# Optimization experiments

Measured on AMD Instinct MI355X. Metric: run time of the kernel, lower is better.

The kernel has to match this reference:

```python
import jax, jax.numpy as jnp
import numpy as np

B, T, C, H = 4, 2048, 1024, 16
HD = C // H  # head dim = 64


def setup_inputs() -> dict:
    key = jax.random.key(0)
    k1, k2, k3 = jax.random.split(key, 3)
    scale_in = 1.0 / np.sqrt(C)
    return {
        "x": jax.random.normal(k1, (B, T, C), dtype=jnp.float32),
        "W_attn": jax.random.normal(k2, (C, 3 * C), dtype=jnp.float32) * scale_in,
        "b_attn": jnp.zeros((3 * C,), dtype=jnp.float32),
        "W_proj": jax.random.normal(k3, (C, C), dtype=jnp.float32) * scale_in,
        "b_proj": jnp.zeros((C,), dtype=jnp.float32),
    }


def reference(x, W_attn, b_attn, W_proj, b_proj):
    b, t, c = x.shape
    qkv = x @ W_attn + b_attn                      # [B,T,3C]
    q, k, v = jnp.split(qkv, 3, axis=-1)
    # [B,T,C] -> [B,H,T,HD]
    def heads(z):
        return z.reshape(b, t, H, HD).transpose(0, 2, 1, 3)
    q, k, v = heads(q), heads(k), heads(v)
    att = jnp.einsum("bhqd,bhkd->bhqk", q, k) / jnp.sqrt(jnp.float32(HD))
    causal = jnp.tril(jnp.ones((t, t), dtype=bool))
    att = jnp.where(causal, att, -jnp.inf)
    att = jax.nn.softmax(att, axis=-1)             # dropout p=0 -> identity
    y = jnp.einsum("bhqk,bhkd->bhqd", att, v)      # [B,H,T,HD]
    y = y.transpose(0, 2, 1, 3).reshape(b, t, c)   # [B,T,C]
    return y @ W_proj + b_proj
```

## Files before the change

kernel.cpp:

```cpp
#include <hip/hip_runtime.h>
#include <hip/hip_bf16.h>

typedef unsigned int u32;
typedef unsigned short u16;
typedef __bf16 bf16x8 __attribute__((ext_vector_type(8)));
typedef float f32x4 __attribute__((ext_vector_type(4)));
typedef _Float16 f16;
typedef _Float16 f16x2 __attribute__((ext_vector_type(2)));
typedef _Float16 f16x4 __attribute__((ext_vector_type(4)));

#define B_ 4
#define T_ 2048
#define C_ 1024
#define H_ 16
#define HD_ 64
#define M_ (B_*T_)
#define N3C (3*C_)
#define N2C (2*C_)

__device__ __forceinline__ u16 f2bf(float f) {
  u32 u = __builtin_bit_cast(u32, f);
  u = (u + 0x7fffu + ((u >> 16) & 1u)) >> 16;
  return (u16)u;
}

#define GLD16(gp, lp) __builtin_amdgcn_global_load_lds( \
    (const __attribute__((address_space(1))) u32*)(gp), \
    (__attribute__((address_space(3))) u32*)(lp), 16, 0, 0)

#if __has_builtin(__builtin_amdgcn_exp2f)
#define EXP2F(x) __builtin_amdgcn_exp2f(x)
#else
#define EXP2F(x) exp2f(x)
#endif

__global__ __launch_bounds__(256) void prep(
    const float* __restrict__ x, const float* __restrict__ Wa,
    const float* __restrict__ Wp,
    u16* __restrict__ xb, u16* __restrict__ W1t, u16* __restrict__ W2t) {
  __shared__ float t[32][33];
  const int blk = blockIdx.x, tid = threadIdx.x;
  if (blk < 8192) {
    int i = blk * 256 + tid;
    float4 v = ((const float4*)x)[i];
    ushort4 o;
    o.x = f2bf(v.x); o.y = f2bf(v.y); o.z = f2bf(v.z); o.w = f2bf(v.w);
    ((ushort4*)xb)[i] = o;
    return;
  }
  const float* W; u16* Wt; int Ndim, id;
  if (blk < 8192 + 3072) { W = Wa; Wt = W1t; Ndim = N3C; id = blk - 8192; }
  else                   { W = Wp; Wt = W2t; Ndim = C_;  id = blk - 11264; }
  const int nt = Ndim / 32;
  const int n0 = (id % nt) * 32, k0 = (id / nt) * 32;
  const int tx = tid & 31, ty = tid >> 5;
  #pragma unroll
  for (int i = ty; i < 32; i += 8)
    t[i][tx] = W[(long)(k0 + i) * Ndim + n0 + tx];
  __syncthreads();
  #pragma unroll
  for (int i = ty; i < 32; i += 8)
    Wt[(long)(n0 + i) * C_ + k0 + tx] = f2bf(t[tx][i]);
}

__global__ __launch_bounds__(256) void gemm_qkv(
    const u16* __restrict__ A, const u16* __restrict__ Bt,
    const float* __restrict__ bias, u16* __restrict__ qkout,
    f16* __restrict__ vt) {
  __shared__ u16 As[128 * 64];
  __shared__ u16 Bs[128 * 64];
  const int tid = threadIdx.x;
  const int wave = tid >> 6, lane = tid & 63;
  const int wm = wave >> 1, wn = wave & 1;
  const int l15 = lane & 15, quad = lane >> 4;
  const int rA = lane >> 3, cxor = (lane & 7) ^ rA;
  const long rowA0 = (long)blockIdx.x * 128;
  const long colB0 = (long)blockIdx.y * 128;
  const int K = C_;

  f32x4 acc[4][4] = {};

  const u16* Ag = A + (rowA0 + wave * 32 + rA) * K + cxor * 8;
  const u16* Bg = Bt + (colB0 + wave * 32 + rA) * K + cxor * 8;
  u16* Asw = &As[(wave * 32) * 64];
  u16* Bsw = &Bs[(wave * 32) * 64];

  const int fbase = l15 * 64 + ((quad ^ (l15 & 3)) << 3) + (((l15 >> 2) & 1) << 5);
  const int aA0 = wm * 4096 + fbase, aA1 = aA0 ^ 32;
  const int bA0 = wn * 4096 + fbase, bA1 = bA0 ^ 32;

  for (int k0 = 0; k0 < K; k0 += 64) {
    #pragma unroll
    for (int j = 0; j < 4; ++j) {
      GLD16(Ag + (long)j * 8 * K + k0, Asw + j * 8 * 64);
      GLD16(Bg + (long)j * 8 * K + k0, Bsw + j * 8 * 64);
    }
    __syncthreads();
    #pragma unroll
    for (int kk = 0; kk < 2; ++kk) {
      const int ai = kk ? aA1 : aA0;
      const int bi = kk ? bA1 : bA0;
      bf16x8 af[4], bfr[4];
      #pragma unroll
      for (int mt = 0; mt < 4; ++mt)
        af[mt] = *(const bf16x8*)&As[ai + mt * 1024];
      #pragma unroll
      for (int nt = 0; nt < 4; ++nt)
        bfr[nt] = *(const bf16x8*)&Bs[bi + nt * 1024];
      #pragma unroll
      for (int mt = 0; mt < 4; ++mt)
        #pragma unroll
        for (int nt = 0; nt < 4; ++nt)
          acc[mt][nt] = __builtin_amdgcn_mfma_f32_16x16x32_bf16(
              af[mt], bfr[nt], acc[mt][nt], 0, 0, 0);
    }
    __syncthreads();
  }

  float bl[4];
  #pragma unroll
  for (int nt = 0; nt < 4; ++nt)
    bl[nt] = bias[colB0 + wn * 64 + nt * 16 + l15];

  const bool vmode = (colB0 >= N2C);
  #pragma unroll
  for (int mt = 0; mt < 4; ++mt) {
    long row = rowA0 + wm * 64 + mt * 16 + quad * 4;
    #pragma unroll
    for (int nt = 0; nt < 4; ++nt) {
      long col = colB0 + wn * 64 + nt * 16 + l15;
      float v0 = acc[mt][nt][0] + bl[nt];
      float v1 = acc[mt][nt][1] + bl[nt];
      float v2 = acc[mt][nt][2] + bl[nt];
      float v3 = acc[mt][nt][3] + bl[nt];
      if (!vmode) {
        qkout[(row + 0) * N2C + col] = f2bf(v0);
        qkout[(row + 1) * N2C + col] = f2bf(v1);
        qkout[(row + 2) * N2C + col] = f2bf(v2);
        qkout[(row + 3) * N2C + col] = f2bf(v3);
      } else {
        int cv = (int)(col - N2C);
        int hh = cv >> 6, dd = cv & 63;
        int bb = (int)(row >> 11);
        long t = row & 2047;
        f16x2 lo = __builtin_bit_cast(f16x2, __builtin_amdgcn_cvt_pkrtz(v0, v1));
        f16x2 hi = __builtin_bit_cast(f16x2, __builtin_amdgcn_cvt_pkrtz(v2, v3));
        f16x4 w; w[0] = lo[0]; w[1] = lo[1]; w[2] = hi[0]; w[3] = hi[1];
        *(f16x4*)&vt[(((long)bb * H_ + hh) * HD_ + dd) * T_ + t] = w;
      }
    }
  }
}

__global__ __launch_bounds__(256) void gemm_proj(
    const u16* __restrict__ A, const u16* __restrict__ Bt,
    const float* __restrict__ bias, float* __restrict__ Cout) {
  __shared__ u16 As[128 * 64];
  __shared__ u16 Bs[64 * 64];
  const int tid = threadIdx.x;
  const int wave = tid >> 6, lane = tid & 63;
  const int l15 = lane & 15, quad = lane >> 4;
  const int rA = lane >> 3, cxor = (lane & 7) ^ rA;
  const long rowA0 = (long)blockIdx.x * 128;
  const long colB0 = (long)blockIdx.y * 64;
  const int K = C_;

  f32x4 acc[2][4] = {};

  const u16* Ag = A + (rowA0 + wave * 32 + rA) * K + cxor * 8;
  const u16* Bg = Bt + (colB0 + wave * 16 + rA) * K + cxor * 8;
  u16* Asw = &As[(wave * 32) * 64];
  u16* Bsw = &Bs[(wave * 16) * 64];

  const int fbase = l15 * 64 + ((quad ^ (l15 & 3)) << 3) + (((l15 >> 2) & 1) << 5);
  const int aA0 = wave * 2048 + fbase, aA1 = aA0 ^ 32;
  const int bA0 = fbase, bA1 = bA0 ^ 32;

  for (int k0 = 0; k0 < K; k0 += 64) {
    #pragma unroll
    for (int j = 0; j < 4; ++j)
      GLD16(Ag + (long)j * 8 * K + k0, Asw + j * 8 * 64);
    #pragma unroll
    for (int j = 0; j < 2; ++j)
      GLD16(Bg + (long)j * 8 * K + k0, Bsw + j * 8 * 64);
    __syncthreads();
    #pragma unroll
    for (int kk = 0; kk < 2; ++kk) {
      const int ai = kk ? aA1 : aA0;
      const int bi = kk ? bA1 : bA0;
      bf16x8 af[2], bfr[4];
      #pragma unroll
      for (int mt = 0; mt < 2; ++mt)
        af[mt] = *(const bf16x8*)&As[ai + mt * 1024];
      #pragma unroll
      for (int nt = 0; nt < 4; ++nt)
        bfr[nt] = *(const bf16x8*)&Bs[bi + nt * 1024];
      #pragma unroll
      for (int mt = 0; mt < 2; ++mt)
        #pragma unroll
        for (int nt = 0; nt < 4; ++nt)
          acc[mt][nt] = __builtin_amdgcn_mfma_f32_16x16x32_bf16(
              af[mt], bfr[nt], acc[mt][nt], 0, 0, 0);
    }
    __syncthreads();
  }

  float bl[4];
  #pragma unroll
  for (int nt = 0; nt < 4; ++nt)
    bl[nt] = bias[colB0 + nt * 16 + l15];
  #pragma unroll
  for (int mt = 0; mt < 2; ++mt) {
    long row = rowA0 + wave * 32 + mt * 16 + quad * 4;
    #pragma unroll
    for (int nt = 0; nt < 4; ++nt) {
      long col = colB0 + nt * 16 + l15;
      #pragma unroll
      for (int r = 0; r < 4; ++r)
        Cout[(row + r) * C_ + col] = acc[mt][nt][r] + bl[nt];
    }
  }
}

__global__ __launch_bounds__(128) void flash_attn(
    const u16* __restrict__ qk, const f16* __restrict__ vt,
    u16* __restrict__ yb) {
  __shared__ u16 KsF[2 * 64 * 64];
  __shared__ f16 VsF[2 * 64 * 64];
  const int l = blockIdx.x;
  const int bh = l & 63;
  const int qt = 31 - (l >> 6);
  const int b = bh >> 4, h = bh & 15;
  const int tid = threadIdx.x, wave = tid >> 6, lane = tid & 63;
  const int l15 = lane & 15, quad = lane >> 4;
  const int rA = lane >> 3, cxor = (lane & 7) ^ rA;

  const u16* Qb = qk + (long)b * T_ * N2C + h * HD_;
  const f16* Vbase = vt + (long)bh * HD_ * T_;
  const u16* Kb0 = Qb + C_ + (long)(wave * 32 + rA) * N2C + cxor * 8;
  const f16* Vb0 = Vbase + (long)(wave * 32 + rA) * T_ + cxor * 8;

  u16* ksw0 = &KsF[(wave * 32) * 64];
  u16* ksw1 = &KsF[4096 + (wave * 32) * 64];
  f16* vsw0 = &VsF[(wave * 32) * 64];
  f16* vsw1 = &VsF[4096 + (wave * 32) * 64];

  const int kA0 = l15 * 64 + ((quad ^ (l15 & 3)) << 3) + (((l15 >> 2) & 1) << 5);
  const int kA1 = kA0 ^ 32;
  const int vA0 = l15 * 64 + (((quad >> 1) ^ (l15 & 7)) << 3) + ((quad & 1) << 2);

  const float cs = 0.125f * 1.44269504088896340736f;

#define FA_TILE(KT, BUF) do {                                                  \
    __syncthreads();                         \
    if ((KT) + 1 < nKT) {                                                      \
      u16* kd = (BUF) ? ksw0 : ksw1;                                           \
      f16* vd = (BUF) ? vsw0 : vsw1;                                           \
      GLD16(kp, kd);                                                           \
      GLD16(kp + 8 * N2C, kd + 8 * 64);                                        \
      GLD16(kp + 16 * N2C, kd + 16 * 64);                                      \
      GLD16(kp + 24 * N2C, kd + 24 * 64);                                      \
      GLD16(vp, vd);                                                           \
      GLD16(vp + 8 * T_, vd + 8 * 64);                                         \
      GLD16(vp + 16 * T_, vd + 16 * 64);                                       \
      GLD16(vp + 24 * T_, vd + 24 * 64);                                       \
      kp += 64 * N2C;                                                          \
      vp += 64;                                                                \
    }                                                                          \
    f32x4 St[2][4] = {};                                                       \
    _Pragma("unroll")                                                          \
    for (int kk = 0; kk < 2; ++kk) {                                           \
      const int ki = ((kk ? kA1 : kA0)) + (BUF) * 4096;                        \
      _Pragma("unroll")                                                        \
      for (int mt = 0; mt < 4; ++mt) {                                         \
        bf16x8 kf = *(const bf16x8*)&KsF[ki + mt * 1024];                      \
        St[0][mt] = __builtin_amdgcn_mfma_f32_16x16x32_bf16(                   \
            kf, bq[0][kk], St[0][mt], 0, 0, 0);                                \
        St[1][mt] = __builtin_amdgcn_mfma_f32_16x16x32_bf16(                   \
            kf, bq[1][kk], St[1][mt], 0, 0, 0);                                \
      }                                                                        \
    }                                                                          \
    if ((KT) == qt) {                                                          \
      _Pragma("unroll")                                                        \
      for (int g = 0; g < 2; ++g)                                              \
        _Pragma("unroll")                                                      \
        for (int mt = 0; mt < 4; ++mt)                                         \
          _Pragma("unroll")                                                    \
          for (int r = 0; r < 4; ++r)                                          \
            if (mt * 16 + quad * 4 + r > wave * 32 + g * 16 + l15)             \
              St[g][mt][r] = -__builtin_inff();                                \
    }                                                                          \
    f16x4 pf[2][4];                                                            \
    _Pragma("unroll")                                                          \
    for (int g = 0; g < 2; ++g) {                                              \
      float ps = 0.f;                                                          \
      _Pragma("unroll")                                                        \
      for (int mt = 0; mt < 4; ++mt) {                                         \
        float p0 = EXP2F(__builtin_fmaf(St[g][mt][0], cs, nref[g]));           \
        float p1 = EXP2F(__builtin_fmaf(St[g][mt][1], cs, nref[g]));           \
        float p2 = EXP2F(__builtin_fmaf(St[g][mt][2], cs, nref[g]));           \
        float p3 = EXP2F(__builtin_fmaf(St[g][mt][3], cs, nref[g]));           \
        ps += (p0 + p1) + (p2 + p3);                                           \
        f16x2 lo = __builtin_bit_cast(f16x2,                                   \
                                      __builtin_amdgcn_cvt_pkrtz(p0, p1));     \
        f16x2 hi = __builtin_bit_cast(f16x2,                                   \
                                      __builtin_amdgcn_cvt_pkrtz(p2, p3));     \
        pf[g][mt][0] = lo[0]; pf[g][mt][1] = lo[1];                            \
        pf[g][mt][2] = hi[0]; pf[g][mt][3] = hi[1];                            \
      }                                                                        \
      li[g] += ps;                                                             \
    }                                                                          \
    _Pragma("unroll")                                                          \
    for (int kc = 0; kc < 4; ++kc) {                                           \
      const int vi = (vA0 ^ (kc << 4)) + (BUF) * 4096;                         \
      _Pragma("unroll")                                                        \
      for (int dt = 0; dt < 4; ++dt) {                                         \
        f16x4 vf = *(const f16x4*)&VsF[vi + dt * 1024];                        \
        o[0][dt] = __builtin_amdgcn_mfma_f32_16x16x16f16(                      \
            vf, pf[0][kc], o[0][dt], 0, 0, 0);                                 \
        o[1][dt] = __builtin_amdgcn_mfma_f32_16x16x16f16(                      \
            vf, pf[1][kc], o[1][dt], 0, 0, 0);                                 \
      }                                                                        \
    }                                                                          \
  } while (0)

  const int nKT = qt + 1;
  bf16x8 bq[2][2];
  float nref[2], li[2] = {0.f, 0.f};
  #pragma unroll
  for (int g = 0; g < 2; ++g) {
    const int qrow = qt * 64 + wave * 32 + g * 16 + l15;
    bq[g][0] = *(const bf16x8*)&Qb[(long)qrow * N2C + quad * 8];
    bq[g][1] = *(const bf16x8*)&Qb[(long)qrow * N2C + 32 + quad * 8];
    float qq = 0.f;
    #pragma unroll
    for (int j = 0; j < 8; ++j) {
      float a = (float)bq[g][0][j], bv = (float)bq[g][1][j];
      qq = __builtin_fmaf(a, a, qq);
      qq = __builtin_fmaf(bv, bv, qq);
    }
    qq += __shfl_xor(qq, 16);
    qq += __shfl_xor(qq, 32);
    nref[g] = -qq * cs;
  }

  const u16* kp = Kb0;
  const f16* vp = Vb0;

  GLD16(kp, ksw0);
  GLD16(kp + 8 * N2C, ksw0 + 8 * 64);
  GLD16(kp + 16 * N2C, ksw0 + 16 * 64);
  GLD16(kp + 24 * N2C, ksw0 + 24 * 64);
  GLD16(vp, vsw0);
  GLD16(vp + 8 * T_, vsw0 + 8 * 64);
  GLD16(vp + 16 * T_, vsw0 + 16 * 64);
  GLD16(vp + 24 * T_, vsw0 + 24 * 64);
  kp += 64 * N2C;
  vp += 64;

  f32x4 o[2][4] = {};

  int kt = 0;
  #pragma unroll 1
  for (; kt + 1 < nKT; kt += 2) {
    FA_TILE(kt, 0);
    FA_TILE(kt + 1, 1);
  }
  if (nKT & 1) FA_TILE(nKT - 1, 0);

  #pragma unroll
  for (int g = 0; g < 2; ++g) {
    li[g] += __shfl_xor(li[g], 16);
    li[g] += __shfl_xor(li[g], 32);
    float inv = 1.f / li[g];
    const long qrow = qt * 64 + wave * 32 + g * 16 + l15;
    #pragma unroll
    for (int dt = 0; dt < 4; ++dt) {
      ushort4 w;
      w.x = f2bf(o[g][dt][0] * inv);
      w.y = f2bf(o[g][dt][1] * inv);
      w.z = f2bf(o[g][dt][2] * inv);
      w.w = f2bf(o[g][dt][3] * inv);
      *(ushort4*)&yb[((long)b * T_ + qrow) * C_ + h * HD_ + dt * 16 + quad * 4] = w;
    }
  }
#undef FA_TILE
}

extern "C" void kernel_launch(void* const* d_in, const int* in_sizes, int n_in,
                              void* d_out, int out_size, void* d_ws, size_t ws_size,
                              hipStream_t stream) {
  const float* x      = (const float*)d_in[0];
  const float* W_attn = (const float*)d_in[1];
  const float* b_attn = (const float*)d_in[2];
  const float* W_proj = (const float*)d_in[3];
  const float* b_proj = (const float*)d_in[4];
  float* out = (float*)d_out;

  char* ws = (char*)d_ws;
  u16* xb   = (u16*)(ws);
  u16* W1t  = (u16*)(ws + 16777216);
  u16* W2t  = (u16*)(ws + 23068672);
  u16* qkb  = (u16*)(ws + 25165824);
  f16* vtb  = (f16*)(ws + 58720256);
  u16* yb   = (u16*)(ws + 75497472);

  prep<<<dim3(12288), dim3(256), 0, stream>>>(x, W_attn, W_proj, xb, W1t, W2t);
  gemm_qkv<<<dim3(M_ / 128, N3C / 128), dim3(256), 0, stream>>>(
      xb, W1t, b_attn, qkb, vtb);
  flash_attn<<<dim3(2048), dim3(128), 0, stream>>>(qkb, vtb, yb);
  gemm_proj<<<dim3(M_ / 128, C_ / 64), dim3(256), 0, stream>>>(
      yb, W2t, b_proj, out);
}
```

Before: 240.3 us.

## Process two query tiles per flash-attention block with four waves sharing K/V

Each flash-attention block now covers 128 query rows (two 64-row tiles) using four waves of 16 rows each, launching half as many blocks with twice the threads. K/V tiles staged in shared memory are reused by both query groups, which halves global K/V traffic per query row and spreads load work across more waves. The last K tile is handled in a peeled epilogue that only the second query group needs. The trade-offs are coarser work granularity for the causal load balance and an extra masked tile of compute for the first group on the diagonal.

Result: slower. 285.4 us (+18.8%).

```diff
diff --git a/kernel.cpp b/kernel.cpp
--- a/kernel.cpp
+++ b/kernel.cpp
@@ -222,14 +222,14 @@
   }
 }
 
-__global__ __launch_bounds__(128) void flash_attn(
+__global__ __launch_bounds__(256, 4) void flash_attn(
     const u16* __restrict__ qk, const f16* __restrict__ vt,
     u16* __restrict__ yb) {
   __shared__ u16 KsF[2 * 64 * 64];
   __shared__ f16 VsF[2 * 64 * 64];
   const int l = blockIdx.x;
   const int bh = l & 63;
-  const int qt = 31 - (l >> 6);
+  const int p = 15 - (l >> 6);
   const int b = bh >> 4, h = bh & 15;
   const int tid = threadIdx.x, wave = tid >> 6, lane = tid & 63;
   const int l15 = lane & 15, quad = lane >> 4;
@@ -237,19 +237,51 @@
 
   const u16* Qb = qk + (long)b * T_ * N2C + h * HD_;
   const f16* Vbase = vt + (long)bh * HD_ * T_;
-  const u16* Kb0 = Qb + C_ + (long)(wave * 32 + rA) * N2C + cxor * 8;
-  const f16* Vb0 = Vbase + (long)(wave * 32 + rA) * T_ + cxor * 8;
-
-  u16* ksw0 = &KsF[(wave * 32) * 64];
-  u16* ksw1 = &KsF[4096 + (wave * 32) * 64];
-  f16* vsw0 = &VsF[(wave * 32) * 64];
-  f16* vsw1 = &VsF[4096 + (wave * 32) * 64];
+  const u16* Kb0 = Qb + C_ + (long)(wave * 16 + rA) * N2C + cxor * 8;
+  const f16* Vb0 = Vbase + (long)(wave * 16 + rA) * T_ + cxor * 8;
+
+  u16* ksw0 = &KsF[(wave * 16) * 64];
+  u16* ksw1 = &KsF[4096 + (wave * 16) * 64];
+  f16* vsw0 = &VsF[(wave * 16) * 64];
+  f16* vsw1 = &VsF[4096 + (wave * 16) * 64];
 
   const int kA0 = l15 * 64 + ((quad ^ (l15 & 3)) << 3) + (((l15 >> 2) & 1) << 5);
   const int kA1 = kA0 ^ 32;
   const int vA0 = l15 * 64 + (((quad >> 1) ^ (l15 & 7)) << 3) + ((quad & 1) << 2);
 
   const float cs = 0.125f * 1.44269504088896340736f;
+
+  const int nKT = 2 * p + 2;
+  bf16x8 bq[2][2];
+  float nref[2], li[2] = {0.f, 0.f};
+  #pragma unroll
+  for (int g = 0; g < 2; ++g) {
+    const int qrow = p * 128 + g * 64 + wave * 16 + l15;
+    bq[g][0] = *(const bf16x8*)&Qb[(long)qrow * N2C + quad * 8];
+    bq[g][1] = *(const bf16x8*)&Qb[(long)qrow * N2C + 32 + quad * 8];
+    float qq = 0.f;
+    #pragma unroll
+    for (int j = 0; j < 8; ++j) {
+      float a = (float)bq[g][0][j], bv = (float)bq[g][1][j];
+      qq = __builtin_fmaf(a, a, qq);
+      qq = __builtin_fmaf(bv, bv, qq);
+    }
+    qq += __shfl_xor(qq, 16);
+    qq += __shfl_xor(qq, 32);
+    nref[g] = -qq * cs;
+  }
+
+  const u16* kp = Kb0;
+  const f16* vp = Vb0;
+
+  GLD16(kp, ksw0);
+  GLD16(kp + 8 * N2C, ksw0 + 8 * 64);
+  GLD16(vp, vsw0);
+  GLD16(vp + 8 * T_, vsw0 + 8 * 64);
+  kp += 64 * N2C;
+  vp += 64;
+
+  f32x4 o[2][4] = {};
 
 #define FA_TILE(KT, BUF) do {                                                  \
     __syncthreads();                         \
@@ -258,12 +290,8 @@
       f16* vd = (BUF) ? vsw0 : vsw1;                                           \
       GLD16(kp, kd);                                                           \
       GLD16(kp + 8 * N2C, kd + 8 * 64);                                        \
-      GLD16(kp + 16 * N2C, kd + 16 * 64);                                      \
-      GLD16(kp + 24 * N2C, kd + 24 * 64);                                      \
       GLD16(vp, vd);                                                           \
       GLD16(vp + 8 * T_, vd + 8 * 64);                                         \
-      GLD16(vp + 16 * T_, vd + 16 * 64);                                       \
-      GLD16(vp + 24 * T_, vd + 24 * 64);                                       \
       kp += 64 * N2C;                                                          \
       vp += 64;                                                                \
     }                                                                          \
@@ -280,15 +308,13 @@
             kf, bq[1][kk], St[1][mt], 0, 0, 0);                                \
       }                                                                        \
     }                                                                          \
-    if ((KT) == qt) {                                                          \
+    if ((KT) == 2 * p) {                                      \
       _Pragma("unroll")                                                        \
-      for (int g = 0; g < 2; ++g)                                              \
+      for (int mt = 0; mt < 4; ++mt)                                           \
         _Pragma("unroll")                                                      \
-        for (int mt = 0; mt < 4; ++mt)                                         \
-          _Pragma("unroll")                                                    \
-          for (int r = 0; r < 4; ++r)                                          \
-            if (mt * 16 + quad * 4 + r > wave * 32 + g * 16 + l15)             \
-              St[g][mt][r] = -__builtin_inff();                                \
+        for (int r = 0; r < 4; ++r)                                            \
+          if (mt * 16 + quad * 4 + r > wave * 16 + l15)                        \
+            St[0][mt][r] = -__builtin_inff();                                  \
     }                                                                          \
     f16x4 pf[2][4];                                                            \
     _Pragma("unroll")                                                          \
@@ -324,56 +350,66 @@
     }                                                                          \
   } while (0)
 
-  const int nKT = qt + 1;
-  bf16x8 bq[2][2];
-  float nref[2], li[2] = {0.f, 0.f};
-  #pragma unroll
-  for (int g = 0; g < 2; ++g) {
-    const int qrow = qt * 64 + wave * 32 + g * 16 + l15;
-    bq[g][0] = *(const bf16x8*)&Qb[(long)qrow * N2C + quad * 8];
-    bq[g][1] = *(const bf16x8*)&Qb[(long)qrow * N2C + 32 + quad * 8];
-    float qq = 0.f;
-    #pragma unroll
-    for (int j = 0; j < 8; ++j) {
-      float a = (float)bq[g][0][j], bv = (float)bq[g][1][j];
-      qq = __builtin_fmaf(a, a, qq);
-      qq = __builtin_fmaf(bv, bv, qq);
-    }
-    qq += __shfl_xor(qq, 16);
-    qq += __shfl_xor(qq, 32);
-    nref[g] = -qq * cs;
-  }
-
-  const u16* kp = Kb0;
-  const f16* vp = Vb0;
-
-  GLD16(kp, ksw0);
-  GLD16(kp + 8 * N2C, ksw0 + 8 * 64);
-  GLD16(kp + 16 * N2C, ksw0 + 16 * 64);
-  GLD16(kp + 24 * N2C, ksw0 + 24 * 64);
-  GLD16(vp, vsw0);
-  GLD16(vp + 8 * T_, vsw0 + 8 * 64);
-  GLD16(vp + 16 * T_, vsw0 + 16 * 64);
-  GLD16(vp + 24 * T_, vsw0 + 24 * 64);
-  kp += 64 * N2C;
-  vp += 64;
-
-  f32x4 o[2][4] = {};
-
+  const int nMain = 2 * p + 1;
   int kt = 0;
   #pragma unroll 1
-  for (; kt + 1 < nKT; kt += 2) {
+  for (; kt + 1 < nMain; kt += 2) {
     FA_TILE(kt, 0);
     FA_TILE(kt + 1, 1);
   }
-  if (nKT & 1) FA_TILE(nKT - 1, 0);
+  FA_TILE(nMain - 1, 0);
+
+  {
+    __syncthreads();
+    f32x4 St[4] = {};
+    #pragma unroll
+    for (int kk = 0; kk < 2; ++kk) {
+      const int ki = (kk ? kA1 : kA0) + 4096;
+      #pragma unroll
+      for (int mt = 0; mt < 4; ++mt) {
+        bf16x8 kf = *(const bf16x8*)&KsF[ki + mt * 1024];
+        St[mt] = __builtin_amdgcn_mfma_f32_16x16x32_bf16(
+            kf, bq[1][kk], St[mt], 0, 0, 0);
+      }
+    }
+    #pragma unroll
+    for (int mt = 0; mt < 4; ++mt)
+      #pragma unroll
+      for (int r = 0; r < 4; ++r)
+        if (mt * 16 + quad * 4 + r > wave * 16 + l15)
+          St[mt][r] = -__builtin_inff();
+    float ps = 0.f;
+    f16x4 pf[4];
+    #pragma unroll
+    for (int mt = 0; mt < 4; ++mt) {
+      float p0 = EXP2F(__builtin_fmaf(St[mt][0], cs, nref[1]));
+      float p1 = EXP2F(__builtin_fmaf(St[mt][1], cs, nref[1]));
+      float p2 = EXP2F(__builtin_fmaf(St[mt][2], cs, nref[1]));
+      float p3 = EXP2F(__builtin_fmaf(St[mt][3], cs, nref[1]));
+      ps += (p0 + p1) + (p2 + p3);
+      f16x2 lo = __builtin_bit_cast(f16x2, __builtin_amdgcn_cvt_pkrtz(p0, p1));
+      f16x2 hi = __builtin_bit_cast(f16x2, __builtin_amdgcn_cvt_pkrtz(p2, p3));
+      pf[mt][0] = lo[0]; pf[mt][1] = lo[1]; pf[mt][2] = hi[0]; pf[mt][3] = hi[1];
+    }
+    li[1] += ps;
+    #pragma unroll
+    for (int kc = 0; kc < 4; ++kc) {
+      const int vi = (vA0 ^ (kc << 4)) + 4096;
+      #pragma unroll
+      for (int dt = 0; dt < 4; ++dt) {
+        f16x4 vf = *(const f16x4*)&VsF[vi + dt * 1024];
+        o[1][dt] = __builtin_amdgcn_mfma_f32_16x16x16f16(
+            vf, pf[kc], o[1][dt], 0, 0, 0);
+      }
+    }
+  }
 
   #pragma unroll
   for (int g = 0; g < 2; ++g) {
     li[g] += __shfl_xor(li[g], 16);
     li[g] += __shfl_xor(li[g], 32);
     float inv = 1.f / li[g];
-    const long qrow = qt * 64 + wave * 32 + g * 16 + l15;
+    const long qrow = p * 128 + g * 64 + wave * 16 + l15;
     #pragma unroll
     for (int dt = 0; dt < 4; ++dt) {
       ushort4 w;
@@ -408,7 +444,7 @@
   prep<<<dim3(12288), dim3(256), 0, stream>>>(x, W_attn, W_proj, xb, W1t, W2t);
   gemm_qkv<<<dim3(M_ / 128, N3C / 128), dim3(256), 0, stream>>>(
       xb, W1t, b_attn, qkb, vtb);
-  flash_attn<<<dim3(2048), dim3(128), 0, stream>>>(qkb, vtb, yb);
+  flash_attn<<<dim3(1024), dim3(256), 0, stream>>>(qkb, vtb, yb);
   gemm_proj<<<dim3(M_ / 128, C_ / 64), dim3(256), 0, stream>>>(
       yb, W2t, b_proj, out);
 }
```
